# Kernel tuning notes

Hardware: AMD Instinct MI355X
Metric: run time of the kernel (lower is better)

## Reference

```python
import jax, jax.numpy as jnp
import numpy as np

B, N, D = 2, 2048, 1024
H, DH = 16, 64
DI = 4096
EPS = 1e-5
NEG_SLOPE = 0.01  # F.leaky_relu default


def _ln(x, g, b):
    mu = jnp.mean(x, axis=-1, keepdims=True)
    var = jnp.mean((x - mu) ** 2, axis=-1, keepdims=True)
    return (x - mu) * jax.lax.rsqrt(var + EPS) * g + b


def setup_inputs() -> dict:
    key = jax.random.key(0)
    ks = jax.random.split(key, 10)
    s = 0.02
    return {
        "Z": jax.random.normal(ks[0], (B, N, D), jnp.float32),
        "new_mask": jax.random.normal(ks[1], (B, N, N), jnp.float32),
        "mask": jax.random.uniform(ks[2], (B, N, N), jnp.float32),
        "ln1_g": jnp.ones((D,), jnp.float32),
        "ln1_b": jnp.zeros((D,), jnp.float32),
        "qkv_w": jax.random.normal(ks[3], (3 * D, D), jnp.float32) * s,
        "qkv_b": jnp.zeros((3 * D,), jnp.float32),
        "o_w": jax.random.normal(ks[4], (D, H * DH), jnp.float32) * s,
        "ln2_g": jnp.ones((D,), jnp.float32),
        "ln2_b": jnp.zeros((D,), jnp.float32),
        "p1_w": jax.random.normal(ks[5], (DI, D), jnp.float32) * s,
        "p1_b": jnp.zeros((DI,), jnp.float32),
        "p2_w": jax.random.normal(ks[6], (D, DI), jnp.float32) * s,
        "p2_b": jnp.zeros((D,), jnp.float32),
    }


def reference(Z, new_mask, mask, ln1_g, ln1_b, qkv_w, qkv_b, o_w, ln2_g, ln2_b, p1_w, p1_b, p2_w, p2_b):
    inp = Z
    Zn = _ln(Z, ln1_g, ln1_b)
    qkv = (Zn @ qkv_w.T + qkv_b).reshape(B, N, H, 3 * DH)
    # torch chunk order in the source: V, Q, K
    V, Q, K = jnp.split(qkv, 3, axis=3)  # each [B,N,H,DH]
    # scores: einsum('bnij,bmij->binm') == [B,H,N,N]
    W = jnp.einsum("bnhd,bmhd->bhnm", Q, K) / np.sqrt(DH) + new_mask[:, None]
    A = jax.nn.softmax(W, axis=3) * mask[:, None]
    attn = jnp.einsum("bhnm,bmhd->bnhd", A, V).reshape(B, N, D)
    attn = jnp.where(attn >= 0, attn, NEG_SLOPE * attn) @ o_w.T  # leaky_relu then o_net (no bias)
    Z1 = attn + inp
    Zn2 = _ln(Z1, ln2_g, ln2_b)
    h = jax.nn.relu(Zn2 @ p1_w.T + p1_b)
    return h @ p2_w.T + p2_b + Z1
```

## Files before the change

kernel.cpp:

```cpp
#include <hip/hip_runtime.h>

typedef unsigned short u16;
typedef __attribute__((ext_vector_type(8))) short bf16x8;
typedef __attribute__((ext_vector_type(2))) float f32x2;
typedef __attribute__((ext_vector_type(4))) float f32x4;
typedef __attribute__((ext_vector_type(16))) float f32x16;
typedef __attribute__((ext_vector_type(4))) unsigned u32x4;

#define DEV static __device__ __forceinline__

DEV u16 f2bf(float f) {
    unsigned u = __float_as_uint(f);
    u += 0x7FFFu + ((u >> 16) & 1u);
    return (u16)(u >> 16);
}

DEV float uaf(unsigned u) { return __uint_as_float(u); }

typedef const __attribute__((address_space(1))) void* gas1_t;
typedef __attribute__((address_space(3))) void* gas3_t;

DEV void gl_lds16(const u16* g, u16* l) {
    __builtin_amdgcn_global_load_lds((gas1_t)g, (gas3_t)l, 16, 0, 0);
}

DEV unsigned cvtpk_bf16(float a, float b) {
    unsigned r;
    asm("v_cvt_pk_bf16_f32 %0, %1, %2" : "=v"(r) : "v"(a), "v"(b));
    return r;
}

DEV int sw8(int row, int chunk) { return row * 64 + ((chunk ^ (row & 7)) << 3); }

__global__ __launch_bounds__(256) void prep_all(const float* __restrict__ qkv_w,
                                                const float* __restrict__ o_w,
                                                const float* __restrict__ p1_w,
                                                const float* __restrict__ p2_w,
                                                const float* __restrict__ qkv_b,
                                                const float* __restrict__ nm,
                                                const float* __restrict__ pm,
                                                u16* __restrict__ qkvW,
                                                u16* __restrict__ oW,
                                                u16* __restrict__ p1W,
                                                u16* __restrict__ p2W,
                                                float* __restrict__ pbias,
                                                unsigned* __restrict__ Mp) {
    __shared__ uint4 Ls[512];
    const int bid = blockIdx.x, t = threadIdx.x;
    if (bid < 3072) {
        int i = bid * 256 + t;
        int orow = i >> 8, cc = i & 255;
        int region = orow >> 10, rem = orow & 1023, h = rem >> 6, tt = rem & 63;
        int srow = h * 192 + region * 64 + tt;
        float4 v = ((const float4*)qkv_w)[srow * 256 + cc];
        ushort4 o;
        o.x = f2bf(v.x); o.y = f2bf(v.y); o.z = f2bf(v.z); o.w = f2bf(v.w);
        ((ushort4*)qkvW)[i] = o;
    } else if (bid < 4096) {
        int i = (bid - 3072) * 256 + t;
        float4 v = ((const float4*)o_w)[i];
        ushort4 o;
        o.x = f2bf(v.x); o.y = f2bf(v.y); o.z = f2bf(v.z); o.w = f2bf(v.w);
        ((ushort4*)oW)[i] = o;
    } else if (bid < 8192) {
        int i = (bid - 4096) * 256 + t;
        float4 v = ((const float4*)p1_w)[i];
        ushort4 o;
        o.x = f2bf(v.x); o.y = f2bf(v.y); o.z = f2bf(v.z); o.w = f2bf(v.w);
        ((ushort4*)p1W)[i] = o;
    } else if (bid < 12288) {
        int i = (bid - 8192) * 256 + t;
        float4 v = ((const float4*)p2_w)[i];
        ushort4 o;
        o.x = f2bf(v.x); o.y = f2bf(v.y); o.z = f2bf(v.z); o.w = f2bf(v.w);
        ((ushort4*)p2W)[i] = o;
    } else if (bid < 16384) {
        const int idx = bid - 12288;
        const int bb = idx >> 11, r2 = idx & 2047;
        const int mt = r2 >> 5, nt = r2 & 31;
        const int n0 = nt * 64;
        const int n = t >> 2;
        const int mq0 = (t & 3) * 2;
        const size_t fbase = (size_t)bb * 1048576 + (size_t)(n0 + n) * 512 + mt * 8 + mq0;
        const float4 a0 = ((const float4*)nm)[fbase];
        const float4 a1 = ((const float4*)nm)[fbase + 1];
        const float4 b0 = ((const float4*)pm)[fbase];
        const float4 b1 = ((const float4*)pm)[fbase + 1];
        uint4 o0, o1;
        o0.x = ((unsigned)f2bf(b0.x) << 16) | f2bf(a0.x * 1.4426950f);
        o0.y = ((unsigned)f2bf(b0.y) << 16) | f2bf(a0.y * 1.4426950f);
        o0.z = ((unsigned)f2bf(b0.z) << 16) | f2bf(a0.z * 1.4426950f);
        o0.w = ((unsigned)f2bf(b0.w) << 16) | f2bf(a0.w * 1.4426950f);
        o1.x = ((unsigned)f2bf(b1.x) << 16) | f2bf(a1.x * 1.4426950f);
        o1.y = ((unsigned)f2bf(b1.y) << 16) | f2bf(a1.y * 1.4426950f);
        o1.z = ((unsigned)f2bf(b1.z) << 16) | f2bf(a1.z * 1.4426950f);
        o1.w = ((unsigned)f2bf(b1.w) << 16) | f2bf(a1.w * 1.4426950f);
        const int c = mq0 >> 1;
        Ls[c * 128 + n * 2 + 0] = o0;
        Ls[c * 128 + n * 2 + 1] = o1;
        __syncthreads();
        const int wc = t >> 6, j = t & 63;
        const size_t obase = (((size_t)(bb * 64 + mt) * 4) + wc) * 4096 + (size_t)n0 * 2;
        ((uint4*)Mp)[obase + j] = Ls[wc * 128 + j];
        ((uint4*)Mp)[obase + 64 + j] = Ls[wc * 128 + 64 + j];
    } else {
#pragma unroll
        for (int k = 0; k < 12; k++) {
            int i = k * 256 + t;
            int region = i >> 10, rem = i & 1023, h = rem >> 6, tt = rem & 63;
            pbias[i] = qkv_b[h * 192 + region * 64 + tt];
        }
    }
}

__global__ __launch_bounds__(256) void ln_bf16(const float* __restrict__ x,
                                               const float* __restrict__ gam,
                                               const float* __restrict__ bet,
                                               u16* __restrict__ y) {
    const int row = blockIdx.x;
    const int t = threadIdx.x;
    const float4 v = ((const float4*)(x + (size_t)row * 1024))[t];
    float s = v.x + v.y + v.z + v.w;
    float ss = v.x * v.x + v.y * v.y + v.z * v.z + v.w * v.w;
#pragma unroll
    for (int o = 1; o < 64; o <<= 1) {
        s += __shfl_xor(s, o);
        ss += __shfl_xor(ss, o);
    }
    __shared__ float rs[4], rss[4];
    const int wave = t >> 6, lane = t & 63;
    if (lane == 0) { rs[wave] = s; rss[wave] = ss; }
    __syncthreads();
    const float tot = rs[0] + rs[1] + rs[2] + rs[3];
    const float totss = rss[0] + rss[1] + rss[2] + rss[3];
    const float mu = tot * (1.0f / 1024.0f);
    const float var = totss * (1.0f / 1024.0f) - mu * mu;
    const float rstd = rsqrtf(var + 1e-5f);
    const float4 g4 = ((const float4*)gam)[t];
    const float4 b4 = ((const float4*)bet)[t];
    ushort4 o;
    o.x = f2bf((v.x - mu) * rstd * g4.x + b4.x);
    o.y = f2bf((v.y - mu) * rstd * g4.y + b4.y);
    o.z = f2bf((v.z - mu) * rstd * g4.z + b4.z);
    o.w = f2bf((v.w - mu) * rstd * g4.w + b4.w);
    ((ushort4*)(y + (size_t)row * 1024))[t] = o;
}

__global__ __launch_bounds__(256) void ln2_comb4(const float* __restrict__ p0,
                                                 const float* __restrict__ p1,
                                                 const float* __restrict__ p2,
                                                 const float* __restrict__ p3,
                                                 const float* __restrict__ Z,
                                                 const float* __restrict__ gam,
                                                 const float* __restrict__ bet,
                                                 float* __restrict__ Z1,
                                                 u16* __restrict__ y) {
    const int row = blockIdx.x;
    const int t = threadIdx.x;
    const size_t off = (size_t)row * 256 + t;
    const float4 a = ((const float4*)p0)[off];
    const float4 c = ((const float4*)p1)[off];
    const float4 d = ((const float4*)p2)[off];
    const float4 e = ((const float4*)p3)[off];
    const float4 z = ((const float4*)Z)[off];
    float4 v;
    v.x = a.x + c.x + d.x + e.x + z.x;
    v.y = a.y + c.y + d.y + e.y + z.y;
    v.z = a.z + c.z + d.z + e.z + z.z;
    v.w = a.w + c.w + d.w + e.w + z.w;
    ((float4*)Z1)[off] = v;
    float s = v.x + v.y + v.z + v.w;
    float ss = v.x * v.x + v.y * v.y + v.z * v.z + v.w * v.w;
#pragma unroll
    for (int o = 1; o < 64; o <<= 1) {
        s += __shfl_xor(s, o);
        ss += __shfl_xor(ss, o);
    }
    __shared__ float rs[4], rss[4];
    const int wave = t >> 6, lane = t & 63;
    if (lane == 0) { rs[wave] = s; rss[wave] = ss; }
    __syncthreads();
    const float tot = rs[0] + rs[1] + rs[2] + rs[3];
    const float totss = rss[0] + rss[1] + rss[2] + rss[3];
    const float mu = tot * (1.0f / 1024.0f);
    const float var = totss * (1.0f / 1024.0f) - mu * mu;
    const float rstd = rsqrtf(var + 1e-5f);
    const float4 g4 = ((const float4*)gam)[t];
    const float4 b4 = ((const float4*)bet)[t];
    ushort4 o;
    o.x = f2bf((v.x - mu) * rstd * g4.x + b4.x);
    o.y = f2bf((v.y - mu) * rstd * g4.y + b4.y);
    o.z = f2bf((v.z - mu) * rstd * g4.z + b4.z);
    o.w = f2bf((v.w - mu) * rstd * g4.w + b4.w);
    ((ushort4*)(y + (size_t)row * 1024))[t] = o;
}

__global__ __launch_bounds__(256) void out_comb(const float* __restrict__ p0,
                                                const float* __restrict__ p1,
                                                const float* __restrict__ bias,
                                                const float* __restrict__ Z1,
                                                float* __restrict__ out) {
    int i = blockIdx.x * 256 + threadIdx.x;
    float4 a = ((const float4*)p0)[i];
    float4 c = ((const float4*)p1)[i];
    float4 z = ((const float4*)Z1)[i];
    float4 b = ((const float4*)bias)[i & 255];
    float4 o;
    o.x = a.x + c.x + z.x + b.x; o.y = a.y + c.y + z.y + b.y;
    o.z = a.z + c.z + z.z + b.z; o.w = a.w + c.w + z.w + b.w;
    ((float4*)out)[i] = o;
}

template <int EPI>
__global__ __launch_bounds__(256, 3) void gemm_bt(const u16* __restrict__ A,
                                                  const u16* __restrict__ Bt,
                                                  const float* __restrict__ bias,
                                                  void* __restrict__ out0,
                                                  void* __restrict__ out1,
                                                  void* __restrict__ out2,
                                                  int M, int N, int K, int ldk) {
    __shared__ __align__(16) u16 As[2][128 * 32];
    __shared__ __align__(16) u16 Bs[2][128 * 32];
    const int tid = threadIdx.x;
    const int wave = tid >> 6, lane = tid & 63;
    const int lhi = lane >> 4, llo = lane & 15;
    const int gx = gridDim.x;
    const int bid = blockIdx.y * gx + blockIdx.x;
    const int swz = (bid & 7) * ((gx * gridDim.y) >> 3) + (bid >> 3);
    const int bx = swz % gx, by = swz / gx;
    const int kz = blockIdx.z * K;

    const int arow = wave * 32 + (lane >> 2);
    const int asw = ((lane & 3) ^ ((lane >> 2) & 3)) << 3;
    const u16* gA = A + (size_t)(by * 128 + arow) * ldk + kz + asw;
    const u16* gB = Bt + (size_t)(bx * 128 + arow) * ldk + kz + asw;
    u16* lA0 = As[0] + wave * 1024 + lane * 8;
    u16* lA1 = As[1] + wave * 1024 + lane * 8;
    u16* lB0 = Bs[0] + wave * 1024 + lane * 8;
    u16* lB1 = Bs[1] + wave * 1024 + lane * 8;

#define GSTAGE(LA, LB) do { \
        gl_lds16(gA, LA); gl_lds16(gA + 16 * (size_t)ldk, (LA) + 512); \
        gl_lds16(gB, LB); gl_lds16(gB + 16 * (size_t)ldk, (LB) + 512); \
        gA += 32; gB += 32; } while (0)

    const int wr = wave >> 1, wc = wave & 1;
    const f32x4 zero = {0.f, 0.f, 0.f, 0.f};
    f32x4 acc[4][4];
#pragma unroll
    for (int i = 0; i < 4; i++)
#pragma unroll
        for (int j = 0; j < 4; j++) acc[i][j] = zero;

#define GCOMP(AB, BB) do { \
        bf16x8 af[4], bfr[4]; \
        _Pragma("unroll") \
        for (int i = 0; i < 4; i++) { \
            const int r = wr * 64 + i * 16 + llo; \
            af[i] = *(const bf16x8*)((AB) + r * 32 + (((lhi ^ r) & 3) << 3)); \
        } \
        _Pragma("unroll") \
        for (int j = 0; j < 4; j++) { \
            const int r = wc * 64 + j * 16 + llo; \
            bfr[j] = *(const bf16x8*)((BB) + r * 32 + (((lhi ^ r) & 3) << 3)); \
        } \
        __builtin_amdgcn_s_setprio(1); \
        _Pragma("unroll") \
        for (int i = 0; i < 4; i++) \
            _Pragma("unroll") \
            for (int j = 0; j < 4; j++) \
                acc[i][j] = __builtin_amdgcn_mfma_f32_16x16x32_bf16(af[i], bfr[j], acc[i][j], 0, 0, 0); \
        __builtin_amdgcn_s_setprio(0); \
        __syncthreads(); } while (0)

    GSTAGE(lA0, lB0);
    __syncthreads();
    for (int k0 = 0; k0 < K; k0 += 64) {
        if (k0 + 32 < K) GSTAGE(lA1, lB1);
        GCOMP(As[0], Bs[0]);
        if (k0 + 64 < K) GSTAGE(lA0, lB0);
        GCOMP(As[1], Bs[1]);
    }
#undef GCOMP
#undef GSTAGE

    const int rbase = by * 128 + wr * 64 + lhi * 4;
    const int cbase = bx * 128 + wc * 64 + llo;
    float* pout = nullptr;
    if constexpr (EPI == 4) {
        pout = (blockIdx.z < 2) ? ((float*)out0 + (size_t)blockIdx.z * M * N)
                                : ((float*)out1 + (size_t)(blockIdx.z - 2) * M * N);
    }
#pragma unroll
    for (int i = 0; i < 4; i++) {
#pragma unroll
        for (int j = 0; j < 4; j++) {
#pragma unroll
            for (int r = 0; r < 4; r++) {
                const int row = rbase + i * 16 + r;
                const int col = cbase + j * 16;
                float v = acc[i][j][r];
                if constexpr (EPI == 0) {
                    v += bias[col];
                    const int region = col >> 10;
                    const int c = col & 1023;
                    const int b = row >> 11, n = row & 2047;
                    if (region == 0) {
                        ((float*)out0)[(size_t)row * 1024 + c] = v;
                    } else {
                        const int h = c >> 6, t = c & 63;
                        u16* dst = (region == 1) ? (u16*)out1 : (u16*)out2;
                        dst[(((size_t)(b * 16 + h)) * 2048 + n) * 64 + t] = f2bf(v);
                    }
                } else if constexpr (EPI == 2) {
                    v += bias[col];
                    v = v > 0.f ? v : 0.f;
                    ((u16*)out0)[(size_t)row * N + col] = f2bf(v);
                } else {
                    pout[(size_t)row * N + col] = v;
                }
            }
        }
    }
}

__global__ __launch_bounds__(256) void vtrans(const float* __restrict__ Vsc,
                                              u16* __restrict__ Vt) {
    __shared__ u16 Ts[64 * 72];
    const int nt = blockIdx.x;
    const int bh = blockIdx.y;
    const int b = bh >> 4, h = bh & 15;
    const int t = threadIdx.x;
    const int n0 = nt * 64;
    const int nr = t >> 2;
    const int dq = (t & 3) * 16;
    const float* src = Vsc + ((size_t)(b * 2048 + n0 + nr)) * 1024 + h * 64 + dq;
    float4 v0 = ((const float4*)src)[0];
    float4 v1 = ((const float4*)src)[1];
    float4 v2 = ((const float4*)src)[2];
    float4 v3 = ((const float4*)src)[3];
    u16* c0 = Ts + nr;
    c0[(dq + 0) * 72]  = f2bf(v0.x); c0[(dq + 1) * 72]  = f2bf(v0.y);
    c0[(dq + 2) * 72]  = f2bf(v0.z); c0[(dq + 3) * 72]  = f2bf(v0.w);
    c0[(dq + 4) * 72]  = f2bf(v1.x); c0[(dq + 5) * 72]  = f2bf(v1.y);
    c0[(dq + 6) * 72]  = f2bf(v1.z); c0[(dq + 7) * 72]  = f2bf(v1.w);
    c0[(dq + 8) * 72]  = f2bf(v2.x); c0[(dq + 9) * 72]  = f2bf(v2.y);
    c0[(dq + 10) * 72] = f2bf(v2.z); c0[(dq + 11) * 72] = f2bf(v2.w);
    c0[(dq + 12) * 72] = f2bf(v3.x); c0[(dq + 13) * 72] = f2bf(v3.y);
    c0[(dq + 14) * 72] = f2bf(v3.z); c0[(dq + 15) * 72] = f2bf(v3.w);
    __syncthreads();
    const int d = t >> 2, n8 = (t & 3) * 16;
    u16* dstrow = Vt + ((size_t)bh * 64 + d) * 2048 + n0;
#pragma unroll
    for (int w = 0; w < 4; w++) {
        const int gi = (n8 >> 2) + w;
        const int g5 = gi & 7, blk = gi >> 3;
        const int pg = (g5 & 4) | ((g5 & 1) << 1) | ((g5 >> 1) & 1);
        *(uint2*)(dstrow + blk * 32 + pg * 4) = *(const uint2*)(Ts + d * 72 + n8 + w * 4);
    }
}

__global__ __launch_bounds__(256, 4) void attn_fused8(const u16* __restrict__ Qg,
                                                      const u16* __restrict__ Kg,
                                                      const u16* __restrict__ Vtg,
                                                      const unsigned* __restrict__ Mp,
                                                      u16* __restrict__ attnL) {
    __shared__ __align__(16) u16 Ks[2][64 * 64];
    __shared__ __align__(16) u16 Vs[2][64 * 64];
    __shared__ float lsh[2][32], lsh2[2][32];
    const int tid = threadIdx.x, wave = tid >> 6, lane = tid & 63;
    const int qh = wave & 1, wm = wave >> 1;
    const int hi = lane >> 5, l31 = lane & 31;
    const int pid = blockIdx.x;
    const int seq = pid >> 3;
    const int hh = seq & 15;
    const int g = (pid & 7) + (seq >> 4) * 8;
    const int b = g >> 5, qt = g & 31;
    const int bh = b * 16 + hh;
    const int q0 = qt * 64;

    const int l3 = lane >> 3, l7 = lane & 7;
    const int swcol = (l7 ^ l3) << 3;
    const int srow = wave * 16 + l3;
    const u16* kp = Kg + ((size_t)bh * 2048 + srow) * 64 + swcol;
    const u16* vp = Vtg + ((size_t)bh * 64 + srow) * 2048 + swcol;
    u16* lKa = Ks[0] + wave * 1024 + lane * 8;
    u16* lKb = Ks[1] + wave * 1024 + lane * 8;
    u16* lVa = Vs[0] + wave * 1024 + lane * 8;
    u16* lVb = Vs[1] + wave * 1024 + lane * 8;

#define STAGE(LK, LV) do { \
        gl_lds16(kp, LK); gl_lds16(kp + 512, (LK) + 512); \
        gl_lds16(vp, LV); gl_lds16(vp + 16384, (LV) + 512); \
        kp += 4096; vp += 64; } while (0)

    STAGE(lKa, lVa);
    const int qrow = q0 + qh * 32 + l31;
    const u16* qptr = Qg + ((size_t)bh * 2048 + qrow) * 64 + hi * 8;
    bf16x8 qf[4];
#pragma unroll
    for (int ks = 0; ks < 4; ks++) qf[ks] = *(const bf16x8*)(qptr + ks * 16);

    const uint4* mp = (const uint4*)Mp + (size_t)(b * 64 + wm) * 16384
                                       + (size_t)qrow * 2 + hi;

    const f32x16 z16 = {0.f,0.f,0.f,0.f,0.f,0.f,0.f,0.f,0.f,0.f,0.f,0.f,0.f,0.f,0.f,0.f};
    f32x16 accO[2];
    accO[0] = z16; accO[1] = z16;
    f32x2 lsv = {0.f, 0.f};
    const float CS = 0.125f * 1.4426950f;
    const f32x2 csv = {CS, CS};
    __syncthreads();

#define QUAD(M, q) { \
        f32x2 nm0 = {uaf(M.x << 16), uaf(M.y << 16)}; \
        f32x2 nm1 = {uaf(M.z << 16), uaf(M.w << 16)}; \
        const f32x2 sa = {sacc[q], sacc[q + 1]}; \
        const f32x2 sb = {sacc[q + 2], sacc[q + 3]}; \
        nm0 += sa * csv; nm1 += sb * csv; \
        f32x2 e0 = {__builtin_amdgcn_exp2f(nm0.x), __builtin_amdgcn_exp2f(nm0.y)}; \
        f32x2 e1 = {__builtin_amdgcn_exp2f(nm1.x), __builtin_amdgcn_exp2f(nm1.y)}; \
        lsv += e0; lsv += e1; \
        const f32x2 pm0 = {uaf(M.x & 0xFFFF0000u), uaf(M.y & 0xFFFF0000u)}; \
        const f32x2 pm1 = {uaf(M.z & 0xFFFF0000u), uaf(M.w & 0xFFFF0000u)}; \
        e0 *= pm0; e1 *= pm1; \
        wpk[(q) / 2] = cvtpk_bf16(e0.x, e0.y); \
        wpk[(q) / 2 + 1] = cvtpk_bf16(e1.x, e1.y); }

#define ITER(KSB, VSB, LK, LV, DO_STAGE) do { \
        const uint4 M0 = mp[0], M1 = mp[4096], M2 = mp[8192], M3 = mp[12288]; \
        mp += 32768; \
        if (DO_STAGE) STAGE(LK, LV); \
        f32x16 sacc = z16; \
        __builtin_amdgcn_s_setprio(1); \
        _Pragma("unroll") \
        for (int ks = 0; ks < 4; ks++) { \
            const bf16x8 kf = *(const bf16x8*)((KSB) + sw8(wm * 32 + l31, ks * 2 + hi)); \
            sacc = __builtin_amdgcn_mfma_f32_32x32x16_bf16(kf, qf[ks], sacc, 0, 0, 0); \
        } \
        __builtin_amdgcn_s_setprio(0); \
        unsigned wpk[8]; \
        QUAD(M0, 0) QUAD(M1, 4) QUAD(M2, 8) QUAD(M3, 12) \
        const u32x4 fa0v = {wpk[0], wpk[1], wpk[2], wpk[3]}; \
        const u32x4 fa1v = {wpk[4], wpk[5], wpk[6], wpk[7]}; \
        const bf16x8 pa0 = __builtin_bit_cast(bf16x8, fa0v); \
        const bf16x8 pa1 = __builtin_bit_cast(bf16x8, fa1v); \
        __builtin_amdgcn_s_setprio(1); \
        _Pragma("unroll") \
        for (int dh = 0; dh < 2; dh++) { \
            const bf16x8 vf0 = *(const bf16x8*)((VSB) + sw8(dh * 32 + l31, wm * 4 + hi)); \
            accO[dh] = __builtin_amdgcn_mfma_f32_32x32x16_bf16(pa0, vf0, accO[dh], 0, 0, 0); \
            const bf16x8 vf1 = *(const bf16x8*)((VSB) + sw8(dh * 32 + l31, wm * 4 + 2 + hi)); \
            accO[dh] = __builtin_amdgcn_mfma_f32_32x32x16_bf16(pa1, vf1, accO[dh], 0, 0, 0); \
        } \
        __builtin_amdgcn_s_setprio(0); \
        __syncthreads(); } while (0)

    for (int tt = 0; tt < 16; tt++) {
        ITER(Ks[0], Vs[0], lKb, lVb, true);
        ITER(Ks[1], Vs[1], lKa, lVa, (tt < 15));
    }
#undef ITER
#undef QUAD
#undef STAGE

    const float lsum = lsv.x + lsv.y;
    const float lsum2 = lsum + __shfl_xor(lsum, 32);
    float* cb = (float*)&Ks[0][0];
    const int slot = qh * 64 + lane;
    const int s7 = slot & 7;
    if (wm == 1) {
        float* dst = cb + (size_t)slot * 32;
#pragma unroll
        for (int dh = 0; dh < 2; dh++)
#pragma unroll
            for (int c = 0; c < 4; c++) {
                const f32x4 v = {accO[dh][c * 4 + 0], accO[dh][c * 4 + 1],
                                 accO[dh][c * 4 + 2], accO[dh][c * 4 + 3]};
                *(f32x4*)(dst + (((dh * 4 + c) ^ s7) << 2)) = v;
            }
        if (lane < 32) lsh[qh][lane] = lsum2;
    }
    __syncthreads();
    if (wm == 0) {
        const float* src = cb + (size_t)slot * 32;
        const float lt = lsum2 + lsh[qh][l31];
#pragma unroll
        for (int dh = 0; dh < 2; dh++)
#pragma unroll
            for (int c = 0; c < 4; c++) {
                const f32x4 v = *(const f32x4*)(src + (((dh * 4 + c) ^ s7) << 2));
                accO[dh][c * 4 + 0] += v.x;
                accO[dh][c * 4 + 1] += v.y;
                accO[dh][c * 4 + 2] += v.z;
                accO[dh][c * 4 + 3] += v.w;
            }
        if (lane < 32) lsh2[qh][lane] = 1.0f / lt;
    }
    __syncthreads();
    if (wm == 0) {
#pragma unroll
        for (int r = 0; r < 16; r++) {
            const int ql = (r & 3) + 8 * (r >> 2) + 4 * hi;
            const float linv = lsh2[qh][ql];
            const int qg = q0 + qh * 32 + ql;
#pragma unroll
            for (int dh = 0; dh < 2; dh++) {
                float v = accO[dh][r] * linv;
                v = v >= 0.f ? v : 0.01f * v;
                attnL[((size_t)b * 2048 + qg) * 1024 + hh * 64 + dh * 32 + l31] = f2bf(v);
            }
        }
    }
}

extern "C" void kernel_launch(void* const* d_in, const int* in_sizes, int n_in,
                              void* d_out, int out_size, void* d_ws, size_t ws_size,
                              hipStream_t stream) {
    const float* Z     = (const float*)d_in[0];
    const float* nmask = (const float*)d_in[1];
    const float* pmask = (const float*)d_in[2];
    const float* ln1_g = (const float*)d_in[3];
    const float* ln1_b = (const float*)d_in[4];
    const float* qkv_w = (const float*)d_in[5];
    const float* qkv_b = (const float*)d_in[6];
    const float* o_w   = (const float*)d_in[7];
    const float* ln2_g = (const float*)d_in[8];
    const float* ln2_b = (const float*)d_in[9];
    const float* p1_w  = (const float*)d_in[10];
    const float* p1_b  = (const float*)d_in[11];
    const float* p2_w  = (const float*)d_in[12];
    const float* p2_b  = (const float*)d_in[13];
    float* out = (float*)d_out;

    char* w = (char*)d_ws;
    auto take = [&](size_t bytes) -> char* {
        char* p = w;
        w += (bytes + 255) & ~(size_t)255;
        return p;
    };
    u16* qkvW   = (u16*)take((size_t)3072 * 1024 * 2);
    u16* oW     = (u16*)take((size_t)1024 * 1024 * 2);
    u16* p1W    = (u16*)take((size_t)4096 * 1024 * 2);
    u16* p2W    = (u16*)take((size_t)1024 * 4096 * 2);
    u16* Zn     = (u16*)take((size_t)4096 * 1024 * 2);
    u16* Qb     = (u16*)take((size_t)32 * 2048 * 64 * 2);
    u16* Kb     = (u16*)take((size_t)32 * 2048 * 64 * 2);
    u16* Vt     = (u16*)take((size_t)32 * 64 * 2048 * 2);
    u16* attnL  = (u16*)take((size_t)4096 * 1024 * 2);
    float* Z1   = (float*)take((size_t)4096 * 1024 * 4);
    u16* hbuf   = (u16*)take((size_t)4096 * 4096 * 2);
    unsigned* Mp = (unsigned*)take((size_t)2 * 2048 * 2048 * 4);
    float* pbias = (float*)take((size_t)3072 * 4);
    float* Vsc    = (float*)hbuf;
    float* part01 = (float*)Mp;
    float* part23 = (float*)hbuf;

    prep_all<<<dim3(16385), 256, 0, stream>>>(qkv_w, o_w, p1_w, p2_w, qkv_b, nmask, pmask,
                                              qkvW, oW, p1W, p2W, pbias, Mp);
    ln_bf16<<<dim3(4096), 256, 0, stream>>>(Z, ln1_g, ln1_b, Zn);
    gemm_bt<0><<<dim3(24, 32), 256, 0, stream>>>(Zn, qkvW, pbias, Vsc, Qb, Kb, 4096, 3072, 1024, 1024);
    vtrans<<<dim3(32, 32), 256, 0, stream>>>(Vsc, Vt);
    attn_fused8<<<dim3(1024), 256, 0, stream>>>(Qb, Kb, Vt, Mp, attnL);
    gemm_bt<4><<<dim3(8, 32, 4), 256, 0, stream>>>(attnL, oW, nullptr, part01, part23, nullptr,
                                                   4096, 1024, 256, 1024);
    ln2_comb4<<<dim3(4096), 256, 0, stream>>>(part01, part01 + (size_t)4096 * 1024,
                                              part23, part23 + (size_t)4096 * 1024,
                                              Z, ln2_g, ln2_b, Z1, Zn);
    gemm_bt<2><<<dim3(32, 32), 256, 0, stream>>>(Zn, p1W, p1_b, hbuf, nullptr, nullptr,
                                                 4096, 4096, 1024, 1024);
    gemm_bt<4><<<dim3(8, 32, 2), 256, 0, stream>>>(hbuf, p2W, nullptr, part01, nullptr, nullptr,
                                                   4096, 1024, 2048, 4096);
    out_comb<<<dim3(4096), 256, 0, stream>>>(part01, part01 + (size_t)4096 * 1024, p2_b, Z1, out);
}
```

Measured before the change: 423.0 us.

## Prefetch attention mask one tile ahead and fold bias into MFMA accumulator

The attention kernel now loads the packed mask for the next key tile one iteration early, using two register sets that swap roles, so global mask loads overlap with the current tile's MFMA work. The additive mask is pre-scaled by 8 in the prep kernel and used as the initial value of the score accumulator. The scores and bias then need a single multiply by CS before exp2, instead of a separate fused multiply-add per element. The GEMM launch bound is also raised from 3 to 4 waves per SIMD, which may limit registers and cause spills. The extra prefetch registers also raise register pressure in the attention kernel.

```diff
diff --git a/kernel.cpp b/kernel.cpp
--- a/kernel.cpp
+++ b/kernel.cpp
@@ -87,14 +87,14 @@
         const float4 b0 = ((const float4*)pm)[fbase];
         const float4 b1 = ((const float4*)pm)[fbase + 1];
         uint4 o0, o1;
-        o0.x = ((unsigned)f2bf(b0.x) << 16) | f2bf(a0.x * 1.4426950f);
-        o0.y = ((unsigned)f2bf(b0.y) << 16) | f2bf(a0.y * 1.4426950f);
-        o0.z = ((unsigned)f2bf(b0.z) << 16) | f2bf(a0.z * 1.4426950f);
-        o0.w = ((unsigned)f2bf(b0.w) << 16) | f2bf(a0.w * 1.4426950f);
-        o1.x = ((unsigned)f2bf(b1.x) << 16) | f2bf(a1.x * 1.4426950f);
-        o1.y = ((unsigned)f2bf(b1.y) << 16) | f2bf(a1.y * 1.4426950f);
-        o1.z = ((unsigned)f2bf(b1.z) << 16) | f2bf(a1.z * 1.4426950f);
-        o1.w = ((unsigned)f2bf(b1.w) << 16) | f2bf(a1.w * 1.4426950f);
+        o0.x = ((unsigned)f2bf(b0.x) << 16) | f2bf(a0.x * 8.0f);
+        o0.y = ((unsigned)f2bf(b0.y) << 16) | f2bf(a0.y * 8.0f);
+        o0.z = ((unsigned)f2bf(b0.z) << 16) | f2bf(a0.z * 8.0f);
+        o0.w = ((unsigned)f2bf(b0.w) << 16) | f2bf(a0.w * 8.0f);
+        o1.x = ((unsigned)f2bf(b1.x) << 16) | f2bf(a1.x * 8.0f);
+        o1.y = ((unsigned)f2bf(b1.y) << 16) | f2bf(a1.y * 8.0f);
+        o1.z = ((unsigned)f2bf(b1.z) << 16) | f2bf(a1.z * 8.0f);
+        o1.w = ((unsigned)f2bf(b1.w) << 16) | f2bf(a1.w * 8.0f);
         const int c = mq0 >> 1;
         Ls[c * 128 + n * 2 + 0] = o0;
         Ls[c * 128 + n * 2 + 1] = o1;
@@ -212,7 +212,7 @@
 }
 
 template <int EPI>
-__global__ __launch_bounds__(256, 3) void gemm_bt(const u16* __restrict__ A,
+__global__ __launch_bounds__(256, 4) void gemm_bt(const u16* __restrict__ A,
                                                   const u16* __restrict__ Bt,
                                                   const float* __restrict__ bias,
                                                   void* __restrict__ out0,
@@ -360,7 +360,7 @@
     }
 }
 
-__global__ __launch_bounds__(256, 4) void attn_fused8(const u16* __restrict__ Qg,
+__global__ __launch_bounds__(256, 4) void attn_fused9(const u16* __restrict__ Qg,
                                                       const u16* __restrict__ Kg,
                                                       const u16* __restrict__ Vtg,
                                                       const unsigned* __restrict__ Mp,
@@ -403,6 +403,9 @@
 
     const uint4* mp = (const uint4*)Mp + (size_t)(b * 64 + wm) * 16384
                                        + (size_t)qrow * 2 + hi;
+    uint4 mA0 = mp[0], mA1 = mp[4096], mA2 = mp[8192], mA3 = mp[12288];
+    uint4 mB0, mB1, mB2, mB3;
+    mp += 32768;
 
     const f32x16 z16 = {0.f,0.f,0.f,0.f,0.f,0.f,0.f,0.f,0.f,0.f,0.f,0.f,0.f,0.f,0.f,0.f};
     f32x16 accO[2];
@@ -413,13 +416,10 @@
     __syncthreads();
 
 #define QUAD(M, q) { \
-        f32x2 nm0 = {uaf(M.x << 16), uaf(M.y << 16)}; \
-        f32x2 nm1 = {uaf(M.z << 16), uaf(M.w << 16)}; \
-        const f32x2 sa = {sacc[q], sacc[q + 1]}; \
-        const f32x2 sb = {sacc[q + 2], sacc[q + 3]}; \
-        nm0 += sa * csv; nm1 += sb * csv; \
-        f32x2 e0 = {__builtin_amdgcn_exp2f(nm0.x), __builtin_amdgcn_exp2f(nm0.y)}; \
-        f32x2 e1 = {__builtin_amdgcn_exp2f(nm1.x), __builtin_amdgcn_exp2f(nm1.y)}; \
+        const f32x2 s0 = {sacc[q] * CS, sacc[q + 1] * CS}; \
+        const f32x2 s1 = {sacc[q + 2] * CS, sacc[q + 3] * CS}; \
+        f32x2 e0 = {__builtin_amdgcn_exp2f(s0.x), __builtin_amdgcn_exp2f(s0.y)}; \
+        f32x2 e1 = {__builtin_amdgcn_exp2f(s1.x), __builtin_amdgcn_exp2f(s1.y)}; \
         lsv += e0; lsv += e1; \
         const f32x2 pm0 = {uaf(M.x & 0xFFFF0000u), uaf(M.y & 0xFFFF0000u)}; \
         const f32x2 pm1 = {uaf(M.z & 0xFFFF0000u), uaf(M.w & 0xFFFF0000u)}; \
@@ -427,11 +427,21 @@
         wpk[(q) / 2] = cvtpk_bf16(e0.x, e0.y); \
         wpk[(q) / 2 + 1] = cvtpk_bf16(e1.x, e1.y); }
 
-#define ITER(KSB, VSB, LK, LV, DO_STAGE) do { \
-        const uint4 M0 = mp[0], M1 = mp[4096], M2 = mp[8192], M3 = mp[12288]; \
-        mp += 32768; \
-        if (DO_STAGE) STAGE(LK, LV); \
-        f32x16 sacc = z16; \
+#define ITER(KSB, VSB, LK, LV, MC0, MC1, MC2, MC3, MN0, MN1, MN2, MN3, DO_PF) do { \
+        if (DO_PF) { \
+            MN0 = mp[0]; MN1 = mp[4096]; MN2 = mp[8192]; MN3 = mp[12288]; \
+            mp += 32768; \
+            STAGE(LK, LV); \
+        } \
+        f32x16 sacc; \
+        sacc[0] = uaf(MC0.x << 16); sacc[1] = uaf(MC0.y << 16); \
+        sacc[2] = uaf(MC0.z << 16); sacc[3] = uaf(MC0.w << 16); \
+        sacc[4] = uaf(MC1.x << 16); sacc[5] = uaf(MC1.y << 16); \
+        sacc[6] = uaf(MC1.z << 16); sacc[7] = uaf(MC1.w << 16); \
+        sacc[8] = uaf(MC2.x << 16); sacc[9] = uaf(MC2.y << 16); \
+        sacc[10] = uaf(MC2.z << 16); sacc[11] = uaf(MC2.w << 16); \
+        sacc[12] = uaf(MC3.x << 16); sacc[13] = uaf(MC3.y << 16); \
+        sacc[14] = uaf(MC3.z << 16); sacc[15] = uaf(MC3.w << 16); \
         __builtin_amdgcn_s_setprio(1); \
         _Pragma("unroll") \
         for (int ks = 0; ks < 4; ks++) { \
@@ -440,7 +450,7 @@
         } \
         __builtin_amdgcn_s_setprio(0); \
         unsigned wpk[8]; \
-        QUAD(M0, 0) QUAD(M1, 4) QUAD(M2, 8) QUAD(M3, 12) \
+        QUAD(MC0, 0) QUAD(MC1, 4) QUAD(MC2, 8) QUAD(MC3, 12) \
         const u32x4 fa0v = {wpk[0], wpk[1], wpk[2], wpk[3]}; \
         const u32x4 fa1v = {wpk[4], wpk[5], wpk[6], wpk[7]}; \
         const bf16x8 pa0 = __builtin_bit_cast(bf16x8, fa0v); \
@@ -457,8 +467,8 @@
         __syncthreads(); } while (0)
 
     for (int tt = 0; tt < 16; tt++) {
-        ITER(Ks[0], Vs[0], lKb, lVb, true);
-        ITER(Ks[1], Vs[1], lKa, lVa, (tt < 15));
+        ITER(Ks[0], Vs[0], lKb, lVb, mA0, mA1, mA2, mA3, mB0, mB1, mB2, mB3, true);
+        ITER(Ks[1], Vs[1], lKa, lVa, mB0, mB1, mB2, mB3, mA0, mA1, mA2, mA3, (tt < 15));
     }
 #undef ITER
 #undef QUAD
@@ -561,7 +571,7 @@
     ln_bf16<<<dim3(4096), 256, 0, stream>>>(Z, ln1_g, ln1_b, Zn);
     gemm_bt<0><<<dim3(24, 32), 256, 0, stream>>>(Zn, qkvW, pbias, Vsc, Qb, Kb, 4096, 3072, 1024, 1024);
     vtrans<<<dim3(32, 32), 256, 0, stream>>>(Vsc, Vt);
-    attn_fused8<<<dim3(1024), 256, 0, stream>>>(Qb, Kb, Vt, Mp, attnL);
+    attn_fused9<<<dim3(1024), 256, 0, stream>>>(Qb, Kb, Vt, Mp, attnL);
     gemm_bt<4><<<dim3(8, 32, 4), 256, 0, stream>>>(attnL, oW, nullptr, part01, part23, nullptr,
                                                    4096, 1024, 256, 1024);
     ln2_comb4<<<dim3(4096), 256, 0, stream>>>(part01, part01 + (size_t)4096 * 1024,
```

New measurement: 449.6 us. +6.3%, slower.

## Fold LN1 into prep kernel and halve split-K for output projection

Applied to the files above, without the earlier changes.

The first LayerNorm is moved into the prep_all kernel as extra blocks, removing one kernel launch and letting it run alongside the weight and mask conversion. The o_proj GEMM drops from split-K 4 to split-K 2, so each split covers 512 of K. This halves the partial-sum writes and the reads in the LN2 combine kernel, which now sums two partials instead of four. The cost is fewer blocks (512) for the o_proj GEMM, which may reduce occupancy on the device.

```diff
diff --git a/kernel.cpp b/kernel.cpp
--- a/kernel.cpp
+++ b/kernel.cpp
@@ -39,13 +39,18 @@
                                                 const float* __restrict__ qkv_b,
                                                 const float* __restrict__ nm,
                                                 const float* __restrict__ pm,
+                                                const float* __restrict__ Z,
+                                                const float* __restrict__ ln1_g,
+                                                const float* __restrict__ ln1_b,
                                                 u16* __restrict__ qkvW,
                                                 u16* __restrict__ oW,
                                                 u16* __restrict__ p1W,
                                                 u16* __restrict__ p2W,
                                                 float* __restrict__ pbias,
-                                                unsigned* __restrict__ Mp) {
+                                                unsigned* __restrict__ Mp,
+                                                u16* __restrict__ Zn) {
     __shared__ uint4 Ls[512];
+    __shared__ float rs[4], rss[4];
     const int bid = blockIdx.x, t = threadIdx.x;
     if (bid < 3072) {
         int i = bid * 256 + t;
@@ -103,6 +108,32 @@
         const size_t obase = (((size_t)(bb * 64 + mt) * 4) + wc) * 4096 + (size_t)n0 * 2;
         ((uint4*)Mp)[obase + j] = Ls[wc * 128 + j];
         ((uint4*)Mp)[obase + 64 + j] = Ls[wc * 128 + 64 + j];
+    } else if (bid < 20480) {
+        const int row = bid - 16384;
+        const float4 v = ((const float4*)(Z + (size_t)row * 1024))[t];
+        float s = v.x + v.y + v.z + v.w;
+        float ss = v.x * v.x + v.y * v.y + v.z * v.z + v.w * v.w;
+#pragma unroll
+        for (int o = 1; o < 64; o <<= 1) {
+            s += __shfl_xor(s, o);
+            ss += __shfl_xor(ss, o);
+        }
+        const int wave = t >> 6, lane = t & 63;
+        if (lane == 0) { rs[wave] = s; rss[wave] = ss; }
+        __syncthreads();
+        const float tot = rs[0] + rs[1] + rs[2] + rs[3];
+        const float totss = rss[0] + rss[1] + rss[2] + rss[3];
+        const float mu = tot * (1.0f / 1024.0f);
+        const float var = totss * (1.0f / 1024.0f) - mu * mu;
+        const float rstd = rsqrtf(var + 1e-5f);
+        const float4 g4 = ((const float4*)ln1_g)[t];
+        const float4 b4 = ((const float4*)ln1_b)[t];
+        ushort4 o;
+        o.x = f2bf((v.x - mu) * rstd * g4.x + b4.x);
+        o.y = f2bf((v.y - mu) * rstd * g4.y + b4.y);
+        o.z = f2bf((v.z - mu) * rstd * g4.z + b4.z);
+        o.w = f2bf((v.w - mu) * rstd * g4.w + b4.w);
+        ((ushort4*)(Zn + (size_t)row * 1024))[t] = o;
     } else {
 #pragma unroll
         for (int k = 0; k < 12; k++) {
@@ -113,43 +144,8 @@
     }
 }
 
-__global__ __launch_bounds__(256) void ln_bf16(const float* __restrict__ x,
-                                               const float* __restrict__ gam,
-                                               const float* __restrict__ bet,
-                                               u16* __restrict__ y) {
-    const int row = blockIdx.x;
-    const int t = threadIdx.x;
-    const float4 v = ((const float4*)(x + (size_t)row * 1024))[t];
-    float s = v.x + v.y + v.z + v.w;
-    float ss = v.x * v.x + v.y * v.y + v.z * v.z + v.w * v.w;
-#pragma unroll
-    for (int o = 1; o < 64; o <<= 1) {
-        s += __shfl_xor(s, o);
-        ss += __shfl_xor(ss, o);
-    }
-    __shared__ float rs[4], rss[4];
-    const int wave = t >> 6, lane = t & 63;
-    if (lane == 0) { rs[wave] = s; rss[wave] = ss; }
-    __syncthreads();
-    const float tot = rs[0] + rs[1] + rs[2] + rs[3];
-    const float totss = rss[0] + rss[1] + rss[2] + rss[3];
-    const float mu = tot * (1.0f / 1024.0f);
-    const float var = totss * (1.0f / 1024.0f) - mu * mu;
-    const float rstd = rsqrtf(var + 1e-5f);
-    const float4 g4 = ((const float4*)gam)[t];
-    const float4 b4 = ((const float4*)bet)[t];
-    ushort4 o;
-    o.x = f2bf((v.x - mu) * rstd * g4.x + b4.x);
-    o.y = f2bf((v.y - mu) * rstd * g4.y + b4.y);
-    o.z = f2bf((v.z - mu) * rstd * g4.z + b4.z);
-    o.w = f2bf((v.w - mu) * rstd * g4.w + b4.w);
-    ((ushort4*)(y + (size_t)row * 1024))[t] = o;
-}
-
-__global__ __launch_bounds__(256) void ln2_comb4(const float* __restrict__ p0,
+__global__ __launch_bounds__(256) void ln2_comb2(const float* __restrict__ p0,
                                                  const float* __restrict__ p1,
-                                                 const float* __restrict__ p2,
-                                                 const float* __restrict__ p3,
                                                  const float* __restrict__ Z,
                                                  const float* __restrict__ gam,
                                                  const float* __restrict__ bet,
@@ -160,14 +156,12 @@
     const size_t off = (size_t)row * 256 + t;
     const float4 a = ((const float4*)p0)[off];
     const float4 c = ((const float4*)p1)[off];
-    const float4 d = ((const float4*)p2)[off];
-    const float4 e = ((const float4*)p3)[off];
     const float4 z = ((const float4*)Z)[off];
     float4 v;
-    v.x = a.x + c.x + d.x + e.x + z.x;
-    v.y = a.y + c.y + d.y + e.y + z.y;
-    v.z = a.z + c.z + d.z + e.z + z.z;
-    v.w = a.w + c.w + d.w + e.w + z.w;
+    v.x = a.x + c.x + z.x;
+    v.y = a.y + c.y + z.y;
+    v.z = a.z + c.z + z.z;
+    v.w = a.w + c.w + z.w;
     ((float4*)Z1)[off] = v;
     float s = v.x + v.y + v.z + v.w;
     float ss = v.x * v.x + v.y * v.y + v.z * v.z + v.w * v.w;
@@ -288,8 +282,7 @@
     const int cbase = bx * 128 + wc * 64 + llo;
     float* pout = nullptr;
     if constexpr (EPI == 4) {
-        pout = (blockIdx.z < 2) ? ((float*)out0 + (size_t)blockIdx.z * M * N)
-                                : ((float*)out1 + (size_t)(blockIdx.z - 2) * M * N);
+        pout = (float*)out0 + (size_t)blockIdx.z * M * N;
     }
 #pragma unroll
     for (int i = 0; i < 4; i++) {
@@ -556,16 +549,15 @@
     float* part01 = (float*)Mp;
     float* part23 = (float*)hbuf;
 
-    prep_all<<<dim3(16385), 256, 0, stream>>>(qkv_w, o_w, p1_w, p2_w, qkv_b, nmask, pmask,
-                                              qkvW, oW, p1W, p2W, pbias, Mp);
-    ln_bf16<<<dim3(4096), 256, 0, stream>>>(Z, ln1_g, ln1_b, Zn);
+    prep_all<<<dim3(20481), 256, 0, stream>>>(qkv_w, o_w, p1_w, p2_w, qkv_b, nmask, pmask,
+                                              Z, ln1_g, ln1_b,
+                                              qkvW, oW, p1W, p2W, pbias, Mp, Zn);
     gemm_bt<0><<<dim3(24, 32), 256, 0, stream>>>(Zn, qkvW, pbias, Vsc, Qb, Kb, 4096, 3072, 1024, 1024);
     vtrans<<<dim3(32, 32), 256, 0, stream>>>(Vsc, Vt);
     attn_fused8<<<dim3(1024), 256, 0, stream>>>(Qb, Kb, Vt, Mp, attnL);
-    gemm_bt<4><<<dim3(8, 32, 4), 256, 0, stream>>>(attnL, oW, nullptr, part01, part23, nullptr,
-                                                   4096, 1024, 256, 1024);
-    ln2_comb4<<<dim3(4096), 256, 0, stream>>>(part01, part01 + (size_t)4096 * 1024,
-                                              part23, part23 + (size_t)4096 * 1024,
+    gemm_bt<4><<<dim3(8, 32, 2), 256, 0, stream>>>(attnL, oW, nullptr, part01, nullptr, nullptr,
+                                                   4096, 1024, 512, 1024);
+    ln2_comb2<<<dim3(4096), 256, 0, stream>>>(part01, part01 + (size_t)4096 * 1024,
                                               Z, ln2_g, ln2_b, Z1, Zn);
     gemm_bt<2><<<dim3(32, 32), 256, 0, stream>>>(Zn, p1W, p1_b, hbuf, nullptr, nullptr,
                                                  4096, 4096, 1024, 1024);
```

Result: faster. 408.8 us (-3.4%).
